# Kernel optimization log

Hardware: AMD Instinct MI355X
Metric: run time of the kernel (lower is better)

## Reference

```python
import jax, jax.numpy as jnp
import numpy as np

EPS = 1e-6
NEG = 0.2  # leaky-relu negative slope
OBJ_C = 6

def _knn(x, k):
    # x: [B,3,N] -> [B,N,k] indices of k nearest neighbors (incl. self)
    xx = jnp.sum(x * x, axis=1)
    inner = jnp.einsum('bdn,bdm->bnm', x, x)
    pd = 2.0 * inner - xx[:, :, None] - xx[:, None, :]  # negative sq dist
    return jax.lax.top_k(pd, k)[1]

def _gather_pts(xt, idx):
    # xt [B,N,D], idx [B,N,k] -> [B,N,k,D]
    return xt[jnp.arange(xt.shape[0])[:, None, None], idx]

def _vn_lin(W, x):
    # channel-mixing linear over VN channel dim: x [B,Cin,3,...]
    return jnp.einsum('oc,bc...->bo...', W, x)

def _vn_bn(x, g, b, eps=1e-5):
    # VNBatchNorm with batch statistics on vector norms
    n = jnp.linalg.norm(x, axis=2) + EPS          # [B,C,*spatial]
    axes = (0,) + tuple(range(2, n.ndim))
    m = jnp.mean(n, axes, keepdims=True)
    v = jnp.var(n, axes, keepdims=True)
    shp = (1, -1) + (1,) * (n.ndim - 2)
    nb = g.reshape(shp) * (n - m) / jnp.sqrt(v + eps) + b.reshape(shp)
    return x / n[:, :, None] * nb[:, :, None]

def _vn_leaky(p, d):
    dot = jnp.sum(p * d, axis=2, keepdims=True)
    dsq = jnp.sum(d * d, axis=2, keepdims=True)
    return NEG * p + (1.0 - NEG) * jnp.where(dot >= 0, p, p - (dot / (dsq + EPS)) * d)

def _vn_block(x, wf, wd, g=None, b=None):
    # VNLinearLeakyReLU
    p = _vn_lin(wf, x)
    if g is not None:
        p = _vn_bn(p, g, b)
    return _vn_leaky(p, _vn_lin(wd, x))

def _surface_feature(coord, k):
    # coord [B,3,N] -> [B,3(chan),3(vec),N,k]: (nb-ctr, ctr, nb x ctr)
    idx = _knn(coord, k)
    xt = coord.transpose(0, 2, 1)                                  # [B,N,3]
    nb = _gather_pts(xt, idx)[:, :, :, None, :]                    # [B,N,k,1,3]
    ctr = jnp.broadcast_to(xt[:, :, None, None, :], nb.shape)
    f = jnp.concatenate([nb - ctr, ctr, jnp.cross(nb, ctr, axis=-1)], axis=3)
    return f.transpose(0, 3, 4, 1, 2)

def _neighbor_feature(x, coord, k):
    # x [B,C,3,N], knn over coord -> [B,C,3,N,k]
    B, C, _, N = x.shape
    idx = _knn(coord, k)
    xt = x.reshape(B, C * 3, N).transpose(0, 2, 1)                 # [B,N,C*3]
    f = _gather_pts(xt, idx).reshape(B, N, k, C, 3)
    return f.transpose(0, 3, 4, 1, 2)

def _vn_maxpool_down(x, coord, wd, rate):
    # x [B,C,3,N,k]: stride-subsample points, VN-max over k neighbors
    x = x[:, :, :, ::rate, :]
    coord_d = coord[:, :, ::rate]
    dot = jnp.sum(x * _vn_lin(wd, x), axis=2)                      # [B,C,Nd,k]
    idx = jnp.argmax(dot, axis=-1)
    xm = jnp.take_along_axis(x, idx[:, :, None, :, None], axis=-1)[..., 0]
    return xm, coord_d

def _nearest_index(t, s):
    # t [B,N,3], s [B,M,3] -> argmin sq-dist index [B,N]
    d = jnp.sum(t * t, -1)[:, :, None] - 2.0 * jnp.einsum('bnd,bmd->bnm', t, s) + jnp.sum(s * s, -1)[:, None, :]
    return jnp.argmin(d, axis=-1)

def _index_points(x, idx):
    # x [B,C,3,M], idx [B,N] -> [B,C,3,N]
    xt = x.transpose(0, 3, 1, 2)
    return xt[jnp.arange(x.shape[0])[:, None], idx].transpose(0, 2, 3, 1)

def _conv_bn_relu(x, w, b, g, be, eps=1e-5):
    # 1x1 Conv1d + BatchNorm1d (batch stats) + ReLU
    y = jnp.einsum('oc,bcn->bon', w, x) + b[None, :, None]
    m = jnp.mean(y, (0, 2), keepdims=True)
    v = jnp.var(y, (0, 2), keepdims=True)
    return jax.nn.relu(g[None, :, None] * (y - m) / jnp.sqrt(v + eps) + be[None, :, None])

def _forward(x, norm, cat_id, wf0, wd0, g0, b0, wf1, wd1, g1, b1, wp1, wf2, wd2, g2, b2, wf3, wd3, g3, b3, wp2, wf4, wd4, g4, b4, wv1f, wv1d, wv2f, wv2d, w3, ws1, cb1, sg1, sb1, ws2, cb2, sg2, sb2, ws3, cb3, sg3, sb3):
    B, _, _, N = x.shape
    coord = x.reshape(B, 3, N)
    one_hot = jax.nn.one_hot(cat_id, OBJ_C, dtype=x.dtype)
    x0 = _vn_block(_surface_feature(coord, 20), wf0, wd0, g0, b0).mean(-1)   # [B,42,3,N]
    x1 = _vn_block(x0, wf1, wd1, g1, b1)
    x2, coord2 = _vn_maxpool_down(_neighbor_feature(x1, coord, 4), coord, wp1, 4)
    x2 = _vn_block(x2, wf2, wd2, g2, b2)                                     # [B,84,3,N/4]
    x3 = _vn_block(x2, wf3, wd3, g3, b3)
    x4, coord4 = _vn_maxpool_down(_neighbor_feature(x3, coord2, 4), coord2, wp2, 4)
    x4 = _vn_block(x4, wf4, wd4, g4, b4)                                     # [B,168,3,N/16]
    ct = coord.transpose(0, 2, 1)
    i1 = _nearest_index(ct, coord2.transpose(0, 2, 1))
    i2 = _nearest_index(ct, coord4.transpose(0, 2, 1))
    eqv = jnp.concatenate([x0, x1, _index_points(x2, i1), _index_points(x3, i1), _index_points(x4, i2)], axis=1)  # [B,420,3,N]
    mean_feat = eqv.mean(-1, keepdims=True)                                  # [B,420,3,1]
    z = _vn_block(mean_feat, wv1f, wv1d)
    z = _vn_block(z, wv2f, wv2d)
    z = jnp.einsum('bcvm,kc->bvkm', z, w3)                                   # [B,3,2,1]
    inv_gl = jnp.einsum('bijm,bjkm->bikm', mean_feat, z).reshape(B, -1, 1)   # [B,840,1]
    inv_0 = jnp.broadcast_to(inv_gl, (B, inv_gl.shape[1], N))
    inv_1 = jnp.sum(mean_feat * coord[:, None], axis=2)                      # [B,420,N]
    oh = jnp.broadcast_to(one_hot[:, :, None], (B, OBJ_C, N))
    inv = jnp.concatenate([norm, inv_0, inv_1, oh], axis=1)                  # [B,1267,N]
    inv = _conv_bn_relu(inv, ws1, cb1, sg1, sb1)
    inv = _conv_bn_relu(inv, ws2, cb2, sg2, sb2)
    inv = _conv_bn_relu(inv, ws3, cb3, sg3, sb3)                             # [B,420,N]
    return eqv, mean_feat, inv, inv_gl

def setup_inputs():
    key = jax.random.key(0)
    ki = iter(jax.random.split(key, 40))
    B, N, D = 4, 2048, 42
    def lin(o, c):
        return jax.random.normal(next(ki), (o, c), jnp.float32) / float(np.sqrt(c))
    inp = dict(
        x=jax.random.normal(next(ki), (B, 1, 3, N), jnp.float32),
        norm=jax.random.normal(next(ki), (B, 1, N), jnp.float32),
        cat_id=jax.random.randint(next(ki), (B,), 0, OBJ_C),
        wf0=lin(D, 3), wd0=lin(D, 3), g0=jnp.ones(D), b0=jnp.zeros(D),
        wf1=lin(D, D), wd1=lin(D, D), g1=jnp.ones(D), b1=jnp.zeros(D),
        wp1=lin(D, D),
        wf2=lin(2 * D, D), wd2=lin(2 * D, D), g2=jnp.ones(2 * D), b2=jnp.zeros(2 * D),
        wf3=lin(2 * D, 2 * D), wd3=lin(2 * D, 2 * D), g3=jnp.ones(2 * D), b3=jnp.zeros(2 * D),
        wp2=lin(2 * D, 2 * D),
        wf4=lin(4 * D, 2 * D), wd4=lin(4 * D, 2 * D), g4=jnp.ones(4 * D), b4=jnp.zeros(4 * D),
        wv1f=lin(5 * D, 10 * D), wv1d=lin(5 * D, 10 * D),
        wv2f=lin(2 * D, 5 * D), wv2d=lin(2 * D, 5 * D),
        w3=lin(2, 2 * D),
        ws1=lin(1024, 1267), cb1=jnp.zeros(1024), sg1=jnp.ones(1024), sb1=jnp.zeros(1024),
        ws2=lin(512, 1024), cb2=jnp.zeros(512), sg2=jnp.ones(512), sb2=jnp.zeros(512),
        ws3=lin(420, 512), cb3=jnp.zeros(420), sg3=jnp.ones(420), sb3=jnp.zeros(420),
    )
    return inp

def reference(x, norm, cat_id, wf0, wd0, g0, b0, wf1, wd1, g1, b1, wp1, wf2, wd2, g2, b2, wf3, wd3, g3, b3, wp2, wf4, wd4, g4, b4, wv1f, wv1d, wv2f, wv2d, w3, ws1, cb1, sg1, sb1, ws2, cb2, sg2, sb2, ws3, cb3, sg3, sb3):
    return _forward(x, norm, cat_id, wf0, wd0, g0, b0, wf1, wd1, g1, b1, wp1, wf2, wd2, g2, b2, wf3, wd3, g3, b3, wp2, wf4, wd4, g4, b4, wv1f, wv1d, wv2f, wv2d, w3, ws1, cb1, sg1, sb1, ws2, cb2, sg2, sb2, ws3, cb3, sg3, sb3)
```

## Files before the change

### kernel.cpp

```cpp
#include <hip/hip_runtime.h>
#include <hip/hip_bf16.h>
#include <cstdint>
#include <cstddef>

#define NTOT 2048
#define BTOT 4

typedef short bf16x8 __attribute__((ext_vector_type(8)));
typedef float f32x4 __attribute__((ext_vector_type(4)));

__device__ inline unsigned short f2b(float v) {
    __hip_bfloat16 h = __float2bfloat16(v);
    return *reinterpret_cast<unsigned short*>(&h);
}

static const size_t WS_IDX20 = 0;
static const size_t WS_FS    = 163840;
static const size_t WS_X0    = 1638400;
static const size_t WS_X1    = 3702784;
static const size_t WS_XM2   = 5767168;
static const size_t WS_X2    = 6025216;
static const size_t WS_X3    = 6541312;
static const size_t WS_IDX42 = 7057408;
static const size_t WS_XM4   = 7059456;
static const size_t WS_X4    = 7188480;
static const size_t WS_I1    = 7446528;
static const size_t WS_I2    = 7454720;
static const size_t WS_MF    = 7462912;
static const size_t WS_INVGL = 7467952;
static const size_t WS_STATS = 7471312;
static const size_t WS_CST   = 7472992;
static const size_t WS_CB    = 7480320;
static const size_t WS_AB    = 7484416;
static const size_t WS_W0    = 7496704;
static const size_t WS_Z1    = 7497728;
static const size_t WS_Z2    = 7500288;
static const size_t WS_W2B   = 13378560;
static const size_t WS_W3B   = 13640704;
static const size_t WS_Y1T   = 13771776;
static const size_t WS_Y1B   = 0;
static const size_t WS_Y2T   = 7480320;
static const size_t WS_Y2B   = 4194304;
static const size_t WS_Y3T   = WS_Y1T;

#define ST0_OFF 0
#define ST1_OFF 84
#define ST2_OFF 168
#define ST3_OFF 336
#define ST4_OFF 504
#define CST1_OFF 0
#define CST2_OFF 2048
#define CST3_OFF 3072

#define OUT_EQV   0
#define OUT_MF    10321920
#define OUT_INV   10326960
#define OUT_INVGL 13767600

template <int SLOTS, int K>
__global__ __launch_bounds__(256)
void knn_reg_kernel(const float* __restrict__ coord, int cand_stride, int q_stride,
                    int* __restrict__ out_idx, int q_cnt)
{
#pragma clang fp contract(off)
    constexpr int Q = SLOTS / 8;
    int b = blockIdx.y;
    int wave = threadIdx.x >> 6, lane = threadIdx.x & 63;
    int q = blockIdx.x * 4 + wave;
    if (q >= q_cnt) return;
    int nq = q * q_stride;
    float qx = coord[(b * 3 + 0) * NTOT + nq];
    float qy = coord[(b * 3 + 1) * NTOT + nq];
    float qz = coord[(b * 3 + 2) * NTOT + nq];
    float xxq = qx * qx + qy * qy + qz * qz;
    float v[SLOTS];
#pragma unroll
    for (int j = 0; j < SLOTS; ++j) {
        int mo = (lane + 64 * j) * cand_stride;
        float cx = coord[(b * 3 + 0) * NTOT + mo];
        float cy = coord[(b * 3 + 1) * NTOT + mo];
        float cz = coord[(b * 3 + 2) * NTOT + mo];
        float inner = qx * cx + qy * cy + qz * cz;
        float xxc = cx * cx + cy * cy + cz * cz;
        v[j] = (2.0f * inner - xxq) - xxc;
    }
    float qv[Q]; int qj[Q];
#pragma unroll
    for (int qq = 0; qq < Q; ++qq) {
        float nv = v[qq * 8]; int nj = qq * 8;
#pragma unroll
        for (int j = 1; j < 8; ++j)
            if (v[qq * 8 + j] > nv) { nv = v[qq * 8 + j]; nj = qq * 8 + j; }
        qv[qq] = nv; qj[qq] = nj;
    }
#pragma clang loop unroll(disable)
    for (int kk = 0; kk < K; ++kk) {
        float bv = qv[0]; int bj = qj[0];
#pragma unroll
        for (int qq = 1; qq < Q; ++qq)
            if (qv[qq] > bv) { bv = qv[qq]; bj = qj[qq]; }
        int bm = lane + 64 * bj;
        for (int off = 32; off; off >>= 1) {
            float ov = __shfl_down(bv, off);
            int   om = __shfl_down(bm, off);
            if (ov > bv || (ov == bv && om < bm)) { bv = ov; bm = om; }
        }
        int m_win = __builtin_amdgcn_readfirstlane(bm);
        if (lane == 0)
            out_idx[((size_t)(b * q_cnt) + q) * K + kk] = m_win;
        int w_slot = m_win >> 6;
        bool isw = (lane == (m_win & 63));
#pragma unroll
        for (int qq = 0; qq < Q; ++qq) {
            if (qq == (w_slot >> 3)) {
#pragma unroll
                for (int j = 0; j < 8; ++j)
                    if (qq * 8 + j == w_slot)
                        v[qq * 8 + j] = isw ? -3.4e38f : v[qq * 8 + j];
                float nv = v[qq * 8]; int nj = qq * 8;
#pragma unroll
                for (int j = 1; j < 8; ++j)
                    if (v[qq * 8 + j] > nv) { nv = v[qq * 8 + j]; nj = qq * 8 + j; }
                qv[qq] = nv; qj[qq] = nj;
            }
        }
    }
}

template <int SLOTS>
__global__ __launch_bounds__(256)
void nearest_reg_kernel(const float* __restrict__ coord, int cand_stride,
                        int* __restrict__ out)
{
#pragma clang fp contract(off)
    int b = blockIdx.y;
    int wave = threadIdx.x >> 6, lane = threadIdx.x & 63;
    int n = blockIdx.x * 4 + wave;
    float qx = coord[(b * 3 + 0) * NTOT + n];
    float qy = coord[(b * 3 + 1) * NTOT + n];
    float qz = coord[(b * 3 + 2) * NTOT + n];
    float tt = qx * qx + qy * qy + qz * qz;
    float v[SLOTS];
#pragma unroll
    for (int j = 0; j < SLOTS; ++j) {
        int mo = (lane + 64 * j) * cand_stride;
        float cx = coord[(b * 3 + 0) * NTOT + mo];
        float cy = coord[(b * 3 + 1) * NTOT + mo];
        float cz = coord[(b * 3 + 2) * NTOT + mo];
        float inner = qx * cx + qy * cy + qz * cz;
        float ss = cx * cx + cy * cy + cz * cz;
        v[j] = (tt - 2.0f * inner) + ss;
    }
    float bv = v[0];
    int bj = 0;
#pragma unroll
    for (int j = 1; j < SLOTS; ++j)
        if (v[j] < bv) { bv = v[j]; bj = j; }
    int bm = lane + 64 * bj;
    for (int off = 32; off; off >>= 1) {
        float ov = __shfl_down(bv, off);
        int   om = __shfl_down(bm, off);
        if (ov < bv || (ov == bv && om < bm)) { bv = ov; bm = om; }
    }
    if (lane == 0) out[b * NTOT + n] = bm;
}

__global__ void surf_build_kernel(const float* __restrict__ coord,
                                  const int* __restrict__ idx20,
                                  float* __restrict__ fs)
{
    int t = blockIdx.x * 256 + threadIdx.x;
    if (t >= BTOT * NTOT * 20) return;
    int n = (t / 20) & (NTOT - 1);
    int b = t / (20 * NTOT);
    int m = idx20[t];
    float cx = coord[(b * 3 + 0) * NTOT + n];
    float cy = coord[(b * 3 + 1) * NTOT + n];
    float cz = coord[(b * 3 + 2) * NTOT + n];
    float nx = coord[(b * 3 + 0) * NTOT + m];
    float ny = coord[(b * 3 + 1) * NTOT + m];
    float nz = coord[(b * 3 + 2) * NTOT + m];
    float* f9 = fs + (size_t)t * 9;
    f9[0] = nx - cx; f9[1] = ny - cy; f9[2] = nz - cz;
    f9[3] = cx;      f9[4] = cy;      f9[5] = cz;
    f9[6] = ny * cz - nz * cy;
    f9[7] = nz * cx - nx * cz;
    f9[8] = nx * cy - ny * cx;
}

__global__ __launch_bounds__(256)
void stats0_kernel(const float* __restrict__ fs,
                   const float* __restrict__ wf0,
                   double* __restrict__ stats)
{
    __shared__ float fl[6 * 180];
    __shared__ double red[2][6][42];
    int t = threadIdx.x, b = blockIdx.y;
    int ps = t / 42, o = t - ps * 42;
    bool active = ps < 6;
    float w0 = 0.f, w1 = 0.f, w2 = 0.f;
    if (active) { w0 = wf0[o * 3]; w1 = wf0[o * 3 + 1]; w2 = wf0[o * 3 + 2]; }
    double s = 0.0, s2 = 0.0;
    int base = blockIdx.x * 48;
    for (int it = 0; it < 8; ++it) {
        int n0 = base + it * 6;
        __syncthreads();
        for (int i = t; i < 1080; i += 256) {
            int pl = i / 180, off = i - pl * 180;
            int n = n0 + pl; if (n > NTOT - 1) n = NTOT - 1;
            fl[i] = fs[((size_t)(b * NTOT + n) * 20) * 9 + off];
        }
        __syncthreads();
        if (active && n0 + ps < NTOT) {
            const float* f = &fl[ps * 180];
            for (int k = 0; k < 20; ++k) {
                const float* f9 = &f[k * 9];
                float p0 = w0 * f9[0] + w1 * f9[3] + w2 * f9[6];
                float p1 = w0 * f9[1] + w1 * f9[4] + w2 * f9[7];
                float p2 = w0 * f9[2] + w1 * f9[5] + w2 * f9[8];
                float nrm = sqrtf(p0 * p0 + p1 * p1 + p2 * p2) + 1e-6f;
                s += (double)nrm; s2 += (double)nrm * (double)nrm;
            }
        }
    }
    if (active) { red[0][ps][o] = s; red[1][ps][o] = s2; }
    __syncthreads();
    if (t < 42) {
        double a = 0.0, a2 = 0.0;
#pragma unroll
        for (int p = 0; p < 6; ++p) { a += red[0][p][t]; a2 += red[1][p][t]; }
        atomicAdd(&stats[t], a);
        atomicAdd(&stats[42 + t], a2);
    }
}

__global__ __launch_bounds__(256)
void apply0_kernel(const float* __restrict__ fs,
                   const float* __restrict__ wf0,
                   const float* __restrict__ wd0,
                   const float* __restrict__ g0,
                   const float* __restrict__ b0,
                   const double* __restrict__ stats,
                   float* __restrict__ x0)
{
    __shared__ float fl[6 * 180];
    int t = threadIdx.x;
    int b = blockIdx.y;
    int ps = t / 42, o = t - ps * 42;
    int n0 = blockIdx.x * 6;
    for (int i = t; i < 1080; i += 256) {
        int pl = i / 180, off = i - pl * 180;
        int n = n0 + pl; if (n > NTOT - 1) n = NTOT - 1;
        fl[i] = fs[((size_t)(b * NTOT + n) * 20) * 9 + off];
    }
    __syncthreads();
    int n = n0 + ps;
    if (ps >= 6 || n >= NTOT) return;
    double S1 = stats[o], S2 = stats[42 + o];
    double md = S1 / 163840.0;
    float m = (float)md;
    float var = (float)(S2 / 163840.0 - md * md);
    float gs = g0[o] / sqrtf(var + 1e-5f);
    float bb = b0[o];
    float wa0 = wf0[o * 3], wa1 = wf0[o * 3 + 1], wa2 = wf0[o * 3 + 2];
    float wb0 = wd0[o * 3], wb1 = wd0[o * 3 + 1], wb2 = wd0[o * 3 + 2];
    float a0 = 0.f, a1 = 0.f, a2 = 0.f;
    const float* f = &fl[ps * 180];
    for (int k = 0; k < 20; ++k) {
        const float* f9 = &f[k * 9];
        float p0 = wa0 * f9[0] + wa1 * f9[3] + wa2 * f9[6];
        float p1 = wa0 * f9[1] + wa1 * f9[4] + wa2 * f9[7];
        float p2 = wa0 * f9[2] + wa1 * f9[5] + wa2 * f9[8];
        float d0 = wb0 * f9[0] + wb1 * f9[3] + wb2 * f9[6];
        float d1 = wb0 * f9[1] + wb1 * f9[4] + wb2 * f9[7];
        float d2 = wb0 * f9[2] + wb1 * f9[5] + wb2 * f9[8];
        float nrm = sqrtf(p0 * p0 + p1 * p1 + p2 * p2) + 1e-6f;
        float nb = gs * (nrm - m) + bb;
        float sc = nb / nrm;
        p0 *= sc; p1 *= sc; p2 *= sc;
        float dot = p0 * d0 + p1 * d1 + p2 * d2;
        float dsq = d0 * d0 + d1 * d1 + d2 * d2 + 1e-6f;
        float tq = fminf(dot, 0.f) / dsq;
        a0 += 0.2f * p0 + 0.8f * (p0 - tq * d0);
        a1 += 0.2f * p1 + 0.8f * (p1 - tq * d1);
        a2 += 0.2f * p2 + 0.8f * (p2 - tq * d2);
    }
    x0[((size_t)(b * 42 + o) * 3 + 0) * NTOT + n] = a0 / 20.0f;
    x0[((size_t)(b * 42 + o) * 3 + 1) * NTOT + n] = a1 / 20.0f;
    x0[((size_t)(b * 42 + o) * 3 + 2) * NTOT + n] = a2 / 20.0f;
}

template <int Ci, int Co, int PTS, int NT, int NIT>
__global__ __launch_bounds__(NT)
void vn_stats_kernel(const float* __restrict__ xin,
                     const float* __restrict__ wf,
                     double* __restrict__ stats, int Npts)
{
    constexpr int Ci3 = Ci * 3;
    constexpr int STRIDE = Ci3 + 1;
    __shared__ float col[PTS * STRIDE];
    __shared__ double red[2][PTS][Co];
    int t = threadIdx.x;
    int b = blockIdx.y;
    int ps = t / Co;
    int o = t - ps * Co;
    bool active = ps < PTS;
    double s = 0.0, s2 = 0.0;
    int base = blockIdx.x * (PTS * NIT);
    for (int it = 0; it < NIT; ++it) {
        int pt0 = base + it * PTS;
        __syncthreads();
        for (int i = t; i < PTS * Ci3; i += NT) {
            int pl = i / Ci3, off = i - pl * Ci3;
            int pt = pt0 + pl; if (pt >= Npts) pt = Npts - 1;
            col[pl * STRIDE + off] = xin[(size_t)(b * 3 * Ci + off) * Npts + pt];
        }
        __syncthreads();
        if (active && pt0 + ps < Npts) {
            const float* cl = &col[ps * STRIDE];
            const float* wr = wf + o * Ci;
            float p0 = 0.f, p1 = 0.f, p2 = 0.f;
#pragma unroll
            for (int c = 0; c < Ci; ++c) {
                float w = wr[c];
                p0 += w * cl[3 * c]; p1 += w * cl[3 * c + 1]; p2 += w * cl[3 * c + 2];
            }
            float nrm = sqrtf(p0 * p0 + p1 * p1 + p2 * p2) + 1e-6f;
            s += (double)nrm; s2 += (double)nrm * (double)nrm;
        }
    }
    if (active) { red[0][ps][o] = s; red[1][ps][o] = s2; }
    __syncthreads();
    if (t < Co) {
        double a = 0.0, a2 = 0.0;
#pragma unroll
        for (int p = 0; p < PTS; ++p) { a += red[0][p][t]; a2 += red[1][p][t]; }
        atomicAdd(&stats[t], a);
        atomicAdd(&stats[Co + t], a2);
    }
}

template <int Ci, int Co, int PTS, int NT>
__global__ __launch_bounds__(NT)
void vn_apply_kernel(const float* __restrict__ xin,
                     const float* __restrict__ wf,
                     const float* __restrict__ wd,
                     const float* __restrict__ g,
                     const float* __restrict__ bbp,
                     const double* __restrict__ stats,
                     double count, int Npts,
                     float* __restrict__ xout)
{
    constexpr int Ci3 = Ci * 3;
    constexpr int STRIDE = Ci3 + 1;
    __shared__ float col[PTS * STRIDE];
    int t = threadIdx.x;
    int b = blockIdx.y;
    int ps = t / Co;
    int o = t - ps * Co;
    bool active = ps < PTS;
    float m = 0.f, gs = 0.f, bb = 0.f;
// ... 193 lines not shown
    }
    if (lane == 0) {
        float dot = p0 * d0 + p1 * d1 + p2 * d2;
        float r0, r1, r2;
        if (dot >= 0.f) { r0 = p0; r1 = p1; r2 = p2; }
        else {
            float tq = dot / (d0 * d0 + d1 * d1 + d2 * d2 + 1e-6f);
            r0 = p0 - tq * d0; r1 = p1 - tq * d1; r2 = p2 - tq * d2;
        }
        z2ws[b * 252 + o * 3]     = 0.2f * p0 + 0.8f * r0;
        z2ws[b * 252 + o * 3 + 1] = 0.2f * p1 + 0.8f * r1;
        z2ws[b * 252 + o * 3 + 2] = 0.2f * p2 + 0.8f * r2;
    }
}

__global__ void z3invgl_kernel(const float* __restrict__ mfw,
                               const float* __restrict__ z2ws,
                               const float* __restrict__ w3,
                               float* __restrict__ invgl_ws,
                               float* __restrict__ out_invgl)
{
    __shared__ float z2[252];
    __shared__ float z3[6];
    __shared__ float mf[1260];
    int b = blockIdx.x;
    int t = threadIdx.x;
    for (int i = t; i < 252; i += 256) z2[i] = z2ws[b * 252 + i];
    for (int i = t; i < 1260; i += 256) mf[i] = mfw[b * 1260 + i];
    __syncthreads();
    if (t < 6) {
        int v = t / 2, kt = t % 2;
        float s = 0.f;
        for (int c = 0; c < 84; ++c) s += z2[c * 3 + v] * w3[kt * 84 + c];
        z3[v * 2 + kt] = s;
    }
    __syncthreads();
    for (int i = t; i < 840; i += 256) {
        int ii = i / 2, kt = i % 2;
        float s = mf[ii * 3] * z3[0 + kt] + mf[ii * 3 + 1] * z3[2 + kt] +
                  mf[ii * 3 + 2] * z3[4 + kt];
        invgl_ws[b * 840 + i] = s;
        out_invgl[b * 840 + i] = s;
    }
}

__global__ __launch_bounds__(256)
void conv1_coef_kernel(const float* __restrict__ ws1,
                       const float* __restrict__ invgl,
                       const float* __restrict__ mfw,
                       const int* __restrict__ cat,
                       float* __restrict__ cb, float* __restrict__ ab,
                       float* __restrict__ w0)
{
    int wave = threadIdx.x >> 6, lane = threadIdx.x & 63;
    int o = blockIdx.x * 4 + wave;
    int b = blockIdx.y;
    const float* wr = ws1 + (size_t)o * 1267;
    float s = 0.f;
    for (int j = lane; j < 840; j += 64)
        s += wr[1 + j] * invgl[b * 840 + j];
    float a0 = 0.f, a1 = 0.f, a2 = 0.f;
    for (int i = lane; i < 420; i += 64) {
        float w = wr[841 + i];
        a0 += w * mfw[b * 1260 + i * 3];
        a1 += w * mfw[b * 1260 + i * 3 + 1];
        a2 += w * mfw[b * 1260 + i * 3 + 2];
    }
    for (int off = 32; off; off >>= 1) {
        s  += __shfl_down(s, off);
        a0 += __shfl_down(a0, off);
        a1 += __shfl_down(a1, off);
        a2 += __shfl_down(a2, off);
    }
    if (lane == 0) {
        cb[b * 1024 + o] = s + wr[1261 + cat[b]];
        ab[((size_t)(b * 1024 + o)) * 3 + 0] = a0;
        ab[((size_t)(b * 1024 + o)) * 3 + 1] = a1;
        ab[((size_t)(b * 1024 + o)) * 3 + 2] = a2;
        if (b == 0) w0[o] = wr[0];
    }
}

__global__ __launch_bounds__(256)
void y1_gen_kernel(const float* __restrict__ cb, const float* __restrict__ ab,
                   const float* __restrict__ w0, const float* __restrict__ coord,
                   const float* __restrict__ normv, float* __restrict__ y1t)
{
    int pt = blockIdx.x;
    int b = pt >> 11, n = pt & 2047;
    float cx = coord[(b * 3 + 0) * NTOT + n];
    float cy = coord[(b * 3 + 1) * NTOT + n];
    float cz = coord[(b * 3 + 2) * NTOT + n];
    float nr = normv[b * NTOT + n];
    for (int it = 0; it < 4; ++it) {
        int o = it * 256 + threadIdx.x;
        size_t bo = (size_t)(b * 1024 + o);
        float v = cb[bo] + ab[bo * 3] * cx + ab[bo * 3 + 1] * cy +
                  ab[bo * 3 + 2] * cz + w0[o] * nr;
        y1t[(size_t)pt * 1024 + o] = v;
    }
}

__global__ void wconv_kernel(const float* __restrict__ src, unsigned short* __restrict__ dst,
                             int Msrc, int Ksrc, int Kpad)
{
    int k = blockIdx.x * 256 + threadIdx.x;
    int o = blockIdx.y;
    float v = (o < Msrc && k < Ksrc) ? src[(size_t)o * Ksrc + k] : 0.f;
    dst[(size_t)o * Kpad + k] = f2b(v);
}

__global__ __launch_bounds__(256)
void gemm_mfma_kernel(const unsigned short* __restrict__ A,
                      const unsigned short* __restrict__ Bw,
                      float* __restrict__ C, int K, int Mreal)
{
    __shared__ __align__(16) unsigned short Al[128 * 40];
    __shared__ __align__(16) unsigned short Bl[128 * 40];
    int t = threadIdx.x;
    int r0 = blockIdx.x * 128;
    int c0 = blockIdx.y * 128;
    int w = t >> 6, l = t & 63;
    int wm = w & 1, wn = w >> 1;
    int lm = l & 15, lq = l >> 4;
    f32x4 acc[4][4] = {};
    for (int k0 = 0; k0 < K; k0 += 32) {
        for (int half = 0; half < 2; ++half) {
            int ch = t + half * 256;
            int row = ch >> 2, kc = ch & 3;
            *(uint4*)&Al[row * 40 + kc * 8] =
                *(const uint4*)&A[(size_t)(r0 + row) * K + k0 + kc * 8];
            *(uint4*)&Bl[row * 40 + kc * 8] =
                *(const uint4*)&Bw[(size_t)(c0 + row) * K + k0 + kc * 8];
        }
        __syncthreads();
        bf16x8 af[4], bfr[4];
#pragma unroll
        for (int i = 0; i < 4; ++i)
            af[i] = *(const bf16x8*)&Al[(wm * 64 + i * 16 + lm) * 40 + lq * 8];
#pragma unroll
        for (int j = 0; j < 4; ++j)
            bfr[j] = *(const bf16x8*)&Bl[(wn * 64 + j * 16 + lm) * 40 + lq * 8];
#pragma unroll
        for (int i = 0; i < 4; ++i)
#pragma unroll
            for (int j = 0; j < 4; ++j)
                acc[i][j] = __builtin_amdgcn_mfma_f32_16x16x32_bf16(af[i], bfr[j],
                                                                    acc[i][j], 0, 0, 0);
        __syncthreads();
    }
#pragma unroll
    for (int i = 0; i < 4; ++i) {
#pragma unroll
        for (int j = 0; j < 4; ++j) {
            int col = c0 + wn * 64 + j * 16 + lm;
            if (col < Mreal) {
                int rbase = r0 + wm * 64 + i * 16 + lq * 4;
#pragma unroll
                for (int r = 0; r < 4; ++r)
                    C[(size_t)(rbase + r) * Mreal + col] = acc[i][j][r];
            }
        }
    }
}

__global__ void cstatsT_kernel(const float* __restrict__ Ct, float* __restrict__ st,
                               int Mreal)
{
    __shared__ float l1[256], l2[256];
    int t = threadIdx.x;
    int o = blockIdx.x * 64 + (t & 63);
    int r0 = blockIdx.y * 128 + (t >> 6) * 32;
    float s = 0.f, s2 = 0.f;
    if (o < Mreal) {
        for (int rr = 0; rr < 32; ++rr) {
            float v = Ct[(size_t)(r0 + rr) * Mreal + o];
            s += v; s2 += v * v;
        }
    }
    l1[t] = s; l2[t] = s2;
    __syncthreads();
    if (t < 64 && o < Mreal) {
        s  = l1[t] + l1[t + 64] + l1[t + 128] + l1[t + 192];
        s2 = l2[t] + l2[t + 64] + l2[t + 128] + l2[t + 192];
        atomicAdd(&st[o], s);
        atomicAdd(&st[Mreal + o], s2);
    }
}

__global__ void bnreluT_kernel(const float* __restrict__ Ct, const float* __restrict__ st,
                               const float* __restrict__ g, const float* __restrict__ be,
                               unsigned short* __restrict__ outb, int M, int maskM)
{
    size_t idx = (size_t)blockIdx.x * 256 + threadIdx.x;
    int o = (int)(idx & (size_t)maskM);
    float m = st[o] * (1.f / 8192.f);
    float var = st[M + o] * (1.f / 8192.f) - m * m;
    float sqv = sqrtf(var + 1e-5f);
    float v = g[o] * (Ct[idx] - m) / sqv + be[o];
    outb[idx] = f2b(v > 0.f ? v : 0.f);
}

__global__ void bnrelu_outT_kernel(const float* __restrict__ Ct, const float* __restrict__ st,
                                   const float* __restrict__ g, const float* __restrict__ be,
                                   float* __restrict__ outinv)
{
    __shared__ float tile[64][65];
    int t = threadIdx.x;
    int r0 = blockIdx.x * 64;
    int o0 = blockIdx.y * 64;
    int b = r0 >> 11, n0 = r0 & 2047;
    int oi = t & 63;
    int o = o0 + oi;
    float m = 0.f, sqv = 1.f, gg = 0.f, bb = 0.f;
    if (o < 420) {
        m = st[o] * (1.f / 8192.f);
        float var = st[420 + o] * (1.f / 8192.f) - m * m;
        sqv = sqrtf(var + 1e-5f);
        gg = g[o]; bb = be[o];
    }
    for (int it = 0; it < 16; ++it) {
        int rr = it * 4 + (t >> 6);
        float v = 0.f;
        if (o < 420) {
            v = gg * (Ct[(size_t)(r0 + rr) * 420 + o] - m) / sqv + bb;
            v = v > 0.f ? v : 0.f;
        }
        tile[rr][oi] = v;
    }
    __syncthreads();
    for (int it = 0; it < 16; ++it) {
        int oc = it * 4 + (t >> 6);
        int oo = o0 + oc;
        if (oo < 420)
            outinv[((size_t)(b * 420 + oo)) * 2048 + n0 + (t & 63)] = tile[t & 63][oc];
    }
}

extern "C" void kernel_launch(void* const* d_in, const int* in_sizes, int n_in,
                              void* d_out, int out_size, void* d_ws, size_t ws_size,
                              hipStream_t stream)
{
    (void)in_sizes; (void)n_in; (void)out_size; (void)ws_size;
    const float* xc   = (const float*)d_in[0];
    const float* normv= (const float*)d_in[1];
    const int*   cat  = (const int*)d_in[2];
    const float* wf0  = (const float*)d_in[3];
    const float* wd0  = (const float*)d_in[4];
    const float* g0   = (const float*)d_in[5];
    const float* b0   = (const float*)d_in[6];
    const float* wf1  = (const float*)d_in[7];
    const float* wd1  = (const float*)d_in[8];
    const float* g1   = (const float*)d_in[9];
    const float* b1   = (const float*)d_in[10];
    const float* wp1  = (const float*)d_in[11];
    const float* wf2  = (const float*)d_in[12];
    const float* wd2  = (const float*)d_in[13];
    const float* g2   = (const float*)d_in[14];
    const float* b2   = (const float*)d_in[15];
    const float* wf3  = (const float*)d_in[16];
    const float* wd3  = (const float*)d_in[17];
    const float* g3   = (const float*)d_in[18];
    const float* b3   = (const float*)d_in[19];
    const float* wp2  = (const float*)d_in[20];
    const float* wf4  = (const float*)d_in[21];
    const float* wd4  = (const float*)d_in[22];
    const float* g4   = (const float*)d_in[23];
    const float* b4   = (const float*)d_in[24];
    const float* wv1f = (const float*)d_in[25];
    const float* wv1d = (const float*)d_in[26];
    const float* wv2f = (const float*)d_in[27];
    const float* wv2d = (const float*)d_in[28];
    const float* w3   = (const float*)d_in[29];
    const float* ws1  = (const float*)d_in[30];
    const float* sg1  = (const float*)d_in[32];
    const float* sb1  = (const float*)d_in[33];
    const float* ws2  = (const float*)d_in[34];
    const float* sg2  = (const float*)d_in[36];
    const float* sb2  = (const float*)d_in[37];
    const float* ws3  = (const float*)d_in[38];
    const float* sg3  = (const float*)d_in[40];
    const float* sb3  = (const float*)d_in[41];

    float* ws = (float*)d_ws;
    float* out = (float*)d_out;

    int*    idx20 = (int*)(ws + WS_IDX20);
    float*  fs    = ws + WS_FS;
    float*  x0    = ws + WS_X0;
    float*  x1    = ws + WS_X1;
    float*  xm2   = ws + WS_XM2;
    float*  x2    = ws + WS_X2;
    float*  x3    = ws + WS_X3;
    int*    idx42 = (int*)(ws + WS_IDX42);
    float*  xm4   = ws + WS_XM4;
    float*  x4    = ws + WS_X4;
    int*    i1p   = (int*)(ws + WS_I1);
    int*    i2p   = (int*)(ws + WS_I2);
    float*  mfw   = ws + WS_MF;
    float*  invgl = ws + WS_INVGL;
    double* st    = (double*)(ws + WS_STATS);
    float*  cst   = ws + WS_CST;
    float*  cb    = ws + WS_CB;
    float*  ab    = ws + WS_AB;
    float*  w0    = ws + WS_W0;
    float*  z1ws  = ws + WS_Z1;
    float*  z2ws  = ws + WS_Z2;
    unsigned short* w2b  = (unsigned short*)(ws + WS_W2B);
    unsigned short* w3b  = (unsigned short*)(ws + WS_W3B);
    float*  y1t   = ws + WS_Y1T;
    unsigned short* y1b  = (unsigned short*)(ws + WS_Y1B);
    float*  y2t   = ws + WS_Y2T;
    unsigned short* y2b  = (unsigned short*)(ws + WS_Y2B);
    float*  y3t   = ws + WS_Y3T;

    hipMemsetAsync((void*)st, 0, 840 * sizeof(double), stream);
    hipMemsetAsync((void*)cst, 0, 3912 * sizeof(float), stream);
    hipMemsetAsync((void*)mfw, 0, 5040 * sizeof(float), stream);

    wconv_kernel<<<dim3(4, 512), 256, 0, stream>>>(ws2, w2b, 512, 1024, 1024);
    wconv_kernel<<<dim3(2, 512), 256, 0, stream>>>(ws3, w3b, 420, 512, 512);

    knn_reg_kernel<32, 20><<<dim3(512, 4), 256, 0, stream>>>(xc, 1, 1, idx20, 2048);
    surf_build_kernel<<<640, 256, 0, stream>>>(xc, idx20, fs);

    stats0_kernel<<<dim3(43, 4), 256, 0, stream>>>(fs, wf0, st + ST0_OFF);
    apply0_kernel<<<dim3(342, 4), 256, 0, stream>>>(fs, wf0, wd0, g0, b0,
                                                    st + ST0_OFF, x0);

    vn_stats_kernel<42, 42, 6, 256, 8><<<dim3(43, 4), 256, 0, stream>>>(
        x0, wf1, st + ST1_OFF, 2048);
    vn_apply_kernel<42, 42, 6, 256><<<dim3(342, 4), 256, 0, stream>>>(
        x0, wf1, wd1, g1, b1, st + ST1_OFF, 8192.0, 2048, x1);

    vn_pool_kernel<<<dim3(512, 4), 256, 0, stream>>>(x1, idx20, 40960LL, 80, wp1, xm2,
                                                     42, 2048, 512);
    vn_stats_kernel<42, 84, 3, 256, 8><<<dim3(22, 4), 256, 0, stream>>>(
        xm2, wf2, st + ST2_OFF, 512);
    vn_apply_kernel<42, 84, 3, 256><<<dim3(171, 4), 256, 0, stream>>>(
        xm2, wf2, wd2, g2, b2, st + ST2_OFF, 2048.0, 512, x2);
    vn_stats_kernel<84, 84, 3, 256, 8><<<dim3(22, 4), 256, 0, stream>>>(
        x2, wf3, st + ST3_OFF, 512);
    vn_apply_kernel<84, 84, 3, 256><<<dim3(171, 4), 256, 0, stream>>>(
        x2, wf3, wd3, g3, b3, st + ST3_OFF, 2048.0, 512, x3);

    knn_reg_kernel<8, 4><<<dim3(32, 4), 256, 0, stream>>>(xc, 4, 16, idx42, 128);
    vn_pool_kernel<<<dim3(128, 4), 256, 0, stream>>>(x3, idx42, 512LL, 4, wp2, xm4,
                                                     84, 512, 128);
    vn_stats_kernel<84, 168, 3, 512, 4><<<dim3(11, 4), 512, 0, stream>>>(
        xm4, wf4, st + ST4_OFF, 128);
    vn_apply_kernel<84, 168, 3, 512><<<dim3(43, 4), 512, 0, stream>>>(
        xm4, wf4, wd4, g4, b4, st + ST4_OFF, 512.0, 128, x4);

    nearest_reg_kernel<8><<<dim3(512, 4), 256, 0, stream>>>(xc, 4, i1p);
    nearest_reg_kernel<2><<<dim3(512, 4), 256, 0, stream>>>(xc, 16, i2p);

    eqv_kernel<<<dim3(8, 1260, 4), 256, 0, stream>>>(x0, x1, x2, x3, x4, i1p, i2p,
                                                     out + OUT_EQV, mfw);
    mf_finalize_kernel<<<20, 256, 0, stream>>>(mfw, out + OUT_MF);

    z1_kernel<<<dim3(53, 4), 256, 0, stream>>>(mfw, wv1f, wv1d, z1ws);
    z2_kernel<<<dim3(21, 4), 256, 0, stream>>>(z1ws, wv2f, wv2d, z2ws);
    z3invgl_kernel<<<4, 256, 0, stream>>>(mfw, z2ws, w3, invgl, out + OUT_INVGL);

    conv1_coef_kernel<<<dim3(256, 4), 256, 0, stream>>>(ws1, invgl, mfw, cat, cb, ab, w0);
    y1_gen_kernel<<<8192, 256, 0, stream>>>(cb, ab, w0, xc, normv, y1t);
    cstatsT_kernel<<<dim3(16, 64), 256, 0, stream>>>(y1t, cst + CST1_OFF, 1024);
    bnreluT_kernel<<<32768, 256, 0, stream>>>(y1t, cst + CST1_OFF, sg1, sb1, y1b,
                                              1024, 1023);

    gemm_mfma_kernel<<<dim3(64, 4), 256, 0, stream>>>(y1b, w2b, y2t, 1024, 512);
    cstatsT_kernel<<<dim3(8, 64), 256, 0, stream>>>(y2t, cst + CST2_OFF, 512);
    bnreluT_kernel<<<16384, 256, 0, stream>>>(y2t, cst + CST2_OFF, sg2, sb2, y2b,
                                              512, 511);

    gemm_mfma_kernel<<<dim3(64, 4), 256, 0, stream>>>(y2b, w3b, y3t, 512, 420);
    cstatsT_kernel<<<dim3(7, 64), 256, 0, stream>>>(y3t, cst + CST3_OFF, 420);
    bnrelu_outT_kernel<<<dim3(128, 7), 256, 0, stream>>>(y3t, cst + CST3_OFF, sg3, sb3,
                                                         out + OUT_INV);
}
```

Baseline: 643.4 us.

## Fuse surface features, y1 stats, GEMM column stats; extract top-2 per kNN round

```diff
diff --git a/kernel.cpp b/kernel.cpp
--- a/kernel.cpp
+++ b/kernel.cpp
@@ -57,6 +57,36 @@
 #define OUT_INV   10326960
 #define OUT_INVGL 13767600
 
+__device__ __forceinline__ void merge_pair(float& v1, int& m1, float& v2, int& m2,
+                                           float w1, int n1, float w2, int n2)
+{
+    bool g  = (w1 > v1) || (w1 == v1 && n1 < m1);
+    bool ga = (v1 > w2) || (v1 == w2 && m1 < n2);
+    bool gb = (w1 > v2) || (w1 == v2 && n1 < m2);
+    float s2v = g ? (ga ? v1 : w2) : (gb ? w1 : v2);
+    int   s2m = g ? (ga ? m1 : n2) : (gb ? n1 : m2);
+    float s1v = g ? w1 : v1;
+    int   s1m = g ? n1 : m1;
+    v1 = s1v; m1 = s1m; v2 = s2v; m2 = s2m;
+}
+
+__device__ __forceinline__ void qtop2(const float* v, int base,
+                                      float& a1, int& j1, float& a2, int& j2)
+{
+    a1 = v[base]; j1 = base; a2 = -3.4e38f; j2 = base;
+#pragma unroll
+    for (int j = 1; j < 8; ++j) {
+        float val = v[base + j];
+        bool b1 = val > a1;
+        bool b2 = val > a2;
+        float na2 = b1 ? a1 : (b2 ? val : a2);
+        int   nj2 = b1 ? j1 : (b2 ? base + j : j2);
+        a1 = b1 ? val : a1;
+        j1 = b1 ? base + j : j1;
+        a2 = na2; j2 = nj2;
+    }
+}
+
 template <int SLOTS, int K>
 __global__ __launch_bounds__(256)
 void knn_reg_kernel(const float* __restrict__ coord, int cand_stride, int q_stride,
@@ -84,44 +114,50 @@
         float xxc = cx * cx + cy * cy + cz * cz;
         v[j] = (2.0f * inner - xxq) - xxc;
     }
-    float qv[Q]; int qj[Q];
-#pragma unroll
-    for (int qq = 0; qq < Q; ++qq) {
-        float nv = v[qq * 8]; int nj = qq * 8;
-#pragma unroll
-        for (int j = 1; j < 8; ++j)
-            if (v[qq * 8 + j] > nv) { nv = v[qq * 8 + j]; nj = qq * 8 + j; }
-        qv[qq] = nv; qj[qq] = nj;
-    }
+    float q1v[Q], q2v[Q]; int q1j[Q], q2j[Q];
+#pragma unroll
+    for (int qq = 0; qq < Q; ++qq)
+        qtop2(v, qq * 8, q1v[qq], q1j[qq], q2v[qq], q2j[qq]);
+
 #pragma clang loop unroll(disable)
-    for (int kk = 0; kk < K; ++kk) {
-        float bv = qv[0]; int bj = qj[0];
-#pragma unroll
-        for (int qq = 1; qq < Q; ++qq)
-            if (qv[qq] > bv) { bv = qv[qq]; bj = qj[qq]; }
-        int bm = lane + 64 * bj;
+    for (int r = 0; r < K / 2; ++r) {
+        float b1v, b2v; int b1j, b2j;
+        if constexpr (Q == 4) {
+            float x1v = q1v[0], x2v = q2v[0]; int x1j = q1j[0], x2j = q2j[0];
+            merge_pair(x1v, x1j, x2v, x2j, q1v[1], q1j[1], q2v[1], q2j[1]);
+            float y1v = q1v[2], y2v = q2v[2]; int y1j = q1j[2], y2j = q2j[2];
+            merge_pair(y1v, y1j, y2v, y2j, q1v[3], q1j[3], q2v[3], q2j[3]);
+            merge_pair(x1v, x1j, x2v, x2j, y1v, y1j, y2v, y2j);
+            b1v = x1v; b1j = x1j; b2v = x2v; b2j = x2j;
+        } else {
+            b1v = q1v[0]; b1j = q1j[0]; b2v = q2v[0]; b2j = q2j[0];
+        }
+        int b1m = lane + (b1j << 6);
+        int b2m = lane + (b2j << 6);
         for (int off = 32; off; off >>= 1) {
-            float ov = __shfl_down(bv, off);
-            int   om = __shfl_down(bm, off);
-            if (ov > bv || (ov == bv && om < bm)) { bv = ov; bm = om; }
-        }
-        int m_win = __builtin_amdgcn_readfirstlane(bm);
-        if (lane == 0)
-            out_idx[((size_t)(b * q_cnt) + q) * K + kk] = m_win;
-        int w_slot = m_win >> 6;
-        bool isw = (lane == (m_win & 63));
+            float o1v = __shfl_xor(b1v, off); int o1m = __shfl_xor(b1m, off);
+            float o2v = __shfl_xor(b2v, off); int o2m = __shfl_xor(b2m, off);
+            merge_pair(b1v, b1m, b2v, b2m, o1v, o1m, o2v, o2m);
+        }
+        if (lane == 0) {
+            out_idx[((size_t)(b * q_cnt) + q) * K + 2 * r]     = b1m;
+            out_idx[((size_t)(b * q_cnt) + q) * K + 2 * r + 1] = b2m;
+        }
+        if (r == K / 2 - 1) break;
+        int ws1 = __builtin_amdgcn_readfirstlane(b1m);
+        int ws2 = __builtin_amdgcn_readfirstlane(b2m);
+        int sl1 = ws1 >> 6, sl2 = ws2 >> 6;
+        int wl1 = ws1 & 63, wl2 = ws2 & 63;
 #pragma unroll
         for (int qq = 0; qq < Q; ++qq) {
-            if (qq == (w_slot >> 3)) {
-#pragma unroll
-                for (int j = 0; j < 8; ++j)
-                    if (qq * 8 + j == w_slot)
-                        v[qq * 8 + j] = isw ? -3.4e38f : v[qq * 8 + j];
-                float nv = v[qq * 8]; int nj = qq * 8;
-#pragma unroll
-                for (int j = 1; j < 8; ++j)
-                    if (v[qq * 8 + j] > nv) { nv = v[qq * 8 + j]; nj = qq * 8 + j; }
-                qv[qq] = nv; qj[qq] = nj;
+            if ((sl1 >> 3) == qq || (sl2 >> 3) == qq) {
+#pragma unroll
+                for (int j = 0; j < 8; ++j) {
+                    int sl = qq * 8 + j;
+                    if (sl == sl1) v[sl] = (lane == wl1) ? -3.4e38f : v[sl];
+                    if (sl == sl2) v[sl] = (lane == wl2) ? -3.4e38f : v[sl];
+                }
+                qtop2(v, qq * 8, q1v[qq], q1j[qq], q2v[qq], q2j[qq]);
             }
         }
     }
@@ -165,35 +201,12 @@
     if (lane == 0) out[b * NTOT + n] = bm;
 }
 
-__global__ void surf_build_kernel(const float* __restrict__ coord,
-                                  const int* __restrict__ idx20,
-                                  float* __restrict__ fs)
-{
-    int t = blockIdx.x * 256 + threadIdx.x;
-    if (t >= BTOT * NTOT * 20) return;
-    int n = (t / 20) & (NTOT - 1);
-    int b = t / (20 * NTOT);
-    int m = idx20[t];
-    float cx = coord[(b * 3 + 0) * NTOT + n];
-    float cy = coord[(b * 3 + 1) * NTOT + n];
-    float cz = coord[(b * 3 + 2) * NTOT + n];
-    float nx = coord[(b * 3 + 0) * NTOT + m];
-    float ny = coord[(b * 3 + 1) * NTOT + m];
-    float nz = coord[(b * 3 + 2) * NTOT + m];
-    float* f9 = fs + (size_t)t * 9;
-    f9[0] = nx - cx; f9[1] = ny - cy; f9[2] = nz - cz;
-    f9[3] = cx;      f9[4] = cy;      f9[5] = cz;
-    f9[6] = ny * cz - nz * cy;
-    f9[7] = nz * cx - nx * cz;
-    f9[8] = nx * cy - ny * cx;
-}
-
 __global__ __launch_bounds__(256)
-void stats0_kernel(const float* __restrict__ fs,
-                   const float* __restrict__ wf0,
-                   double* __restrict__ stats)
-{
-    __shared__ float fl[6 * 180];
+void stats0_kernel(const float* __restrict__ coord, const int* __restrict__ idx20,
+                   const float* __restrict__ wf0, double* __restrict__ stats)
+{
+    __shared__ float nbc[360];
+    __shared__ float ctr[18];
     __shared__ double red[2][6][42];
     int t = threadIdx.x, b = blockIdx.y;
     int ps = t / 42, o = t - ps * 42;
@@ -205,19 +218,32 @@
     for (int it = 0; it < 8; ++it) {
         int n0 = base + it * 6;
         __syncthreads();
-        for (int i = t; i < 1080; i += 256) {
-            int pl = i / 180, off = i - pl * 180;
+        if (t < 120) {
+            int pl = t / 20, k = t - pl * 20;
             int n = n0 + pl; if (n > NTOT - 1) n = NTOT - 1;
-            fl[i] = fs[((size_t)(b * NTOT + n) * 20) * 9 + off];
+            int m = idx20[((size_t)(b * NTOT + n)) * 20 + k];
+            nbc[t * 3 + 0] = coord[(b * 3 + 0) * NTOT + m];
+            nbc[t * 3 + 1] = coord[(b * 3 + 1) * NTOT + m];
+            nbc[t * 3 + 2] = coord[(b * 3 + 2) * NTOT + m];
+        }
+        if (t >= 128 && t < 146) {
+            int i = t - 128; int pl = i / 3, vd = i - pl * 3;
+            int n = n0 + pl; if (n > NTOT - 1) n = NTOT - 1;
+            ctr[i] = coord[(b * 3 + vd) * NTOT + n];
         }
         __syncthreads();
         if (active && n0 + ps < NTOT) {
-            const float* f = &fl[ps * 180];
+            float cx = ctr[ps * 3], cy = ctr[ps * 3 + 1], cz = ctr[ps * 3 + 2];
+            const float* nb = &nbc[ps * 60];
             for (int k = 0; k < 20; ++k) {
-                const float* f9 = &f[k * 9];
-                float p0 = w0 * f9[0] + w1 * f9[3] + w2 * f9[6];
-                float p1 = w0 * f9[1] + w1 * f9[4] + w2 * f9[7];
-                float p2 = w0 * f9[2] + w1 * f9[5] + w2 * f9[8];
+                float nx = nb[k * 3], ny = nb[k * 3 + 1], nz = nb[k * 3 + 2];
+                float dx = nx - cx, dy = ny - cy, dz = nz - cz;
+                float crx = ny * cz - nz * cy;
+                float cry = nz * cx - nx * cz;
+                float crz = nx * cy - ny * cx;
+                float p0 = w0 * dx + w1 * cx + w2 * crx;
+                float p1 = w0 * dy + w1 * cy + w2 * cry;
+                float p2 = w0 * dz + w1 * cz + w2 * crz;
                 float nrm = sqrtf(p0 * p0 + p1 * p1 + p2 * p2) + 1e-6f;
                 s += (double)nrm; s2 += (double)nrm * (double)nrm;
             }
@@ -235,23 +261,29 @@
 }
 
 __global__ __launch_bounds__(256)
-void apply0_kernel(const float* __restrict__ fs,
-                   const float* __restrict__ wf0,
-                   const float* __restrict__ wd0,
-                   const float* __restrict__ g0,
-                   const float* __restrict__ b0,
-                   const double* __restrict__ stats,
-                   float* __restrict__ x0)
-{
-    __shared__ float fl[6 * 180];
+void apply0_kernel(const float* __restrict__ coord, const int* __restrict__ idx20,
+                   const float* __restrict__ wf0, const float* __restrict__ wd0,
+                   const float* __restrict__ g0, const float* __restrict__ b0,
+                   const double* __restrict__ stats, float* __restrict__ x0)
+{
+    __shared__ float nbc[360];
+    __shared__ float ctr[18];
     int t = threadIdx.x;
     int b = blockIdx.y;
     int ps = t / 42, o = t - ps * 42;
     int n0 = blockIdx.x * 6;
-    for (int i = t; i < 1080; i += 256) {
-        int pl = i / 180, off = i - pl * 180;
+    if (t < 120) {
+        int pl = t / 20, k = t - pl * 20;
         int n = n0 + pl; if (n > NTOT - 1) n = NTOT - 1;
-        fl[i] = fs[((size_t)(b * NTOT + n) * 20) * 9 + off];
+        int m = idx20[((size_t)(b * NTOT + n)) * 20 + k];
+        nbc[t * 3 + 0] = coord[(b * 3 + 0) * NTOT + m];
+        nbc[t * 3 + 1] = coord[(b * 3 + 1) * NTOT + m];
+        nbc[t * 3 + 2] = coord[(b * 3 + 2) * NTOT + m];
+    }
+    if (t >= 128 && t < 146) {
+        int i = t - 128; int pl = i / 3, vd = i - pl * 3;
+        int n = n0 + pl; if (n > NTOT - 1) n = NTOT - 1;
+        ctr[i] = coord[(b * 3 + vd) * NTOT + n];
     }
     __syncthreads();
     int n = n0 + ps;
@@ -264,19 +296,24 @@
     float bb = b0[o];
     float wa0 = wf0[o * 3], wa1 = wf0[o * 3 + 1], wa2 = wf0[o * 3 + 2];
     float wb0 = wd0[o * 3], wb1 = wd0[o * 3 + 1], wb2 = wd0[o * 3 + 2];
+    float cx = ctr[ps * 3], cy = ctr[ps * 3 + 1], cz = ctr[ps * 3 + 2];
+    const float* nb = &nbc[ps * 60];
     float a0 = 0.f, a1 = 0.f, a2 = 0.f;
-    const float* f = &fl[ps * 180];
     for (int k = 0; k < 20; ++k) {
-        const float* f9 = &f[k * 9];
-        float p0 = wa0 * f9[0] + wa1 * f9[3] + wa2 * f9[6];
-        float p1 = wa0 * f9[1] + wa1 * f9[4] + wa2 * f9[7];
-        float p2 = wa0 * f9[2] + wa1 * f9[5] + wa2 * f9[8];
-        float d0 = wb0 * f9[0] + wb1 * f9[3] + wb2 * f9[6];
-        float d1 = wb0 * f9[1] + wb1 * f9[4] + wb2 * f9[7];
-        float d2 = wb0 * f9[2] + wb1 * f9[5] + wb2 * f9[8];
+        float nx = nb[k * 3], ny = nb[k * 3 + 1], nz = nb[k * 3 + 2];
+        float dx = nx - cx, dy = ny - cy, dz = nz - cz;
+        float crx = ny * cz - nz * cy;
+        float cry = nz * cx - nx * cz;
+        float crz = nx * cy - ny * cx;
+        float p0 = wa0 * dx + wa1 * cx + wa2 * crx;
+        float p1 = wa0 * dy + wa1 * cy + wa2 * cry;
+        float p2 = wa0 * dz + wa1 * cz + wa2 * crz;
+        float d0 = wb0 * dx + wb1 * cx + wb2 * crx;
+        float d1 = wb0 * dy + wb1 * cy + wb2 * cry;
+        float d2 = wb0 * dz + wb1 * cz + wb2 * crz;
         float nrm = sqrtf(p0 * p0 + p1 * p1 + p2 * p2) + 1e-6f;
-        float nb = gs * (nrm - m) + bb;
-        float sc = nb / nrm;
+        float nbv = gs * (nrm - m) + bb;
+        float sc = nbv / nrm;
         p0 *= sc; p1 *= sc; p2 *= sc;
         float dot = p0 * d0 + p1 * d1 + p2 * d2;
         float dsq = d0 * d0 + d1 * d1 + d2 * d2 + 1e-6f;
@@ -636,22 +673,63 @@
 }
 
 __global__ __launch_bounds__(256)
-void y1_gen_kernel(const float* __restrict__ cb, const float* __restrict__ ab,
-                   const float* __restrict__ w0, const float* __restrict__ coord,
-                   const float* __restrict__ normv, float* __restrict__ y1t)
-{
-    int pt = blockIdx.x;
-    int b = pt >> 11, n = pt & 2047;
-    float cx = coord[(b * 3 + 0) * NTOT + n];
-    float cy = coord[(b * 3 + 1) * NTOT + n];
-    float cz = coord[(b * 3 + 2) * NTOT + n];
-    float nr = normv[b * NTOT + n];
-    for (int it = 0; it < 4; ++it) {
-        int o = it * 256 + threadIdx.x;
-        size_t bo = (size_t)(b * 1024 + o);
-        float v = cb[bo] + ab[bo * 3] * cx + ab[bo * 3 + 1] * cy +
-                  ab[bo * 3 + 2] * cz + w0[o] * nr;
-        y1t[(size_t)pt * 1024 + o] = v;
+void y1_stats_kernel(const float* __restrict__ cb, const float* __restrict__ ab,
+                     const float* __restrict__ w0, const float* __restrict__ coord,
+                     const float* __restrict__ normv, float* __restrict__ cst)
+{
+    __shared__ float px[256], py[256], pz[256], pn[256];
+    int t = threadIdx.x;
+    int o = blockIdx.x * 256 + t;
+    int b = blockIdx.y >> 3;
+    int n0 = (blockIdx.y & 7) * 256;
+    px[t] = coord[(b * 3 + 0) * NTOT + n0 + t];
+    py[t] = coord[(b * 3 + 1) * NTOT + n0 + t];
+    pz[t] = coord[(b * 3 + 2) * NTOT + n0 + t];
+    pn[t] = normv[b * NTOT + n0 + t];
+    __syncthreads();
+    size_t bo = (size_t)(b * 1024 + o);
+    float c0 = cb[bo];
+    float a0 = ab[bo * 3], a1 = ab[bo * 3 + 1], a2 = ab[bo * 3 + 2];
+    float wn = w0[o];
+    float s = 0.f, s2 = 0.f;
+    for (int k = 0; k < 256; ++k) {
+        float v = c0 + a0 * px[k] + a1 * py[k] + a2 * pz[k] + wn * pn[k];
+        s += v; s2 += v * v;
+    }
+    atomicAdd(&cst[o], s);
+    atomicAdd(&cst[1024 + o], s2);
+}
+
+__global__ __launch_bounds__(256)
+void y1_bnrelu_kernel(const float* __restrict__ cb, const float* __restrict__ ab,
+                      const float* __restrict__ w0, const float* __restrict__ coord,
+                      const float* __restrict__ normv, const float* __restrict__ cst,
+                      const float* __restrict__ sg, const float* __restrict__ sb,
+                      unsigned short* __restrict__ y1b)
+{
+    __shared__ float px[256], py[256], pz[256], pn[256];
+    int t = threadIdx.x;
+    int o = blockIdx.x * 256 + t;
+    int b = blockIdx.y >> 3;
+    int n0 = (blockIdx.y & 7) * 256;
+    px[t] = coord[(b * 3 + 0) * NTOT + n0 + t];
+    py[t] = coord[(b * 3 + 1) * NTOT + n0 + t];
+    pz[t] = coord[(b * 3 + 2) * NTOT + n0 + t];
+    pn[t] = normv[b * NTOT + n0 + t];
+    __syncthreads();
+    size_t bo = (size_t)(b * 1024 + o);
+    float c0 = cb[bo];
+    float a0 = ab[bo * 3], a1 = ab[bo * 3 + 1], a2 = ab[bo * 3 + 2];
+    float wn = w0[o];
+    float mm = cst[o] * (1.f / 8192.f);
+    float var = cst[1024 + o] * (1.f / 8192.f) - mm * mm;
+    float sc = sg[o] / sqrtf(var + 1e-5f);
+    float bs = sb[o] - mm * sc;
+    size_t rowbase = (size_t)(b * NTOT + n0) * 1024 + o;
+    for (int k = 0; k < 256; ++k) {
+        float v = c0 + a0 * px[k] + a1 * py[k] + a2 * pz[k] + wn * pn[k];
+        float r = sc * v + bs;
+        y1b[rowbase + (size_t)k * 1024] = f2b(r > 0.f ? r : 0.f);
     }
 }
 
@@ -667,11 +745,14 @@
 __global__ __launch_bounds__(256)
 void gemm_mfma_kernel(const unsigned short* __restrict__ A,
                       const unsigned short* __restrict__ Bw,
-                      float* __restrict__ C, int K, int Mreal)
+                      float* __restrict__ C, float* __restrict__ st,
+                      int K, int Mreal)
 {
     __shared__ __align__(16) unsigned short Al[128 * 40];
     __shared__ __align__(16) unsigned short Bl[128 * 40];
+    __shared__ float sst[128], sst2[128];
     int t = threadIdx.x;
+    if (t < 128) { sst[t] = 0.f; sst2[t] = 0.f; }
     int r0 = blockIdx.x * 128;
     int c0 = blockIdx.y * 128;
     int w = t >> 6, l = t & 63;
@@ -716,29 +797,28 @@
             }
         }
     }
-}
-
-__global__ void cstatsT_kernel(const float* __restrict__ Ct, float* __restrict__ st,
-                               int Mreal)
-{
-    __shared__ float l1[256], l2[256];
-    int t = threadIdx.x;
-    int o = blockIdx.x * 64 + (t & 63);
-    int r0 = blockIdx.y * 128 + (t >> 6) * 32;
-    float s = 0.f, s2 = 0.f;
-    if (o < Mreal) {
-        for (int rr = 0; rr < 32; ++rr) {
-            float v = Ct[(size_t)(r0 + rr) * Mreal + o];
-            s += v; s2 += v * v;
-        }
-    }
-    l1[t] = s; l2[t] = s2;
-    __syncthreads();
-    if (t < 64 && o < Mreal) {
-        s  = l1[t] + l1[t + 64] + l1[t + 128] + l1[t + 192];
-        s2 = l2[t] + l2[t + 64] + l2[t + 128] + l2[t + 192];
-        atomicAdd(&st[o], s);
-        atomicAdd(&st[Mreal + o], s2);
+#pragma unroll
+    for (int j = 0; j < 4; ++j) {
+        float s = 0.f, s2 = 0.f;
+#pragma unroll
+        for (int i = 0; i < 4; ++i)
+#pragma unroll
+            for (int r = 0; r < 4; ++r) { float x = acc[i][j][r]; s += x; s2 += x * x; }
+        s  += __shfl_down(s, 32);  s  += __shfl_down(s, 16);
+        s2 += __shfl_down(s2, 32); s2 += __shfl_down(s2, 16);
+        if (l < 16) {
+            int cc = wn * 64 + j * 16 + lm;
+            atomicAdd(&sst[cc], s);
+            atomicAdd(&sst2[cc], s2);
+        }
+    }
+    __syncthreads();
+    if (t < 128) {
+        int col = c0 + t;
+        if (col < Mreal) {
+            atomicAdd(&st[col], sst[t]);
+            atomicAdd(&st[Mreal + col], sst2[t]);
+        }
     }
 }
 
@@ -840,7 +920,6 @@
     float* out = (float*)d_out;
 
     int*    idx20 = (int*)(ws + WS_IDX20);
-    float*  fs    = ws + WS_FS;
     float*  x0    = ws + WS_X0;
     float*  x1    = ws + WS_X1;
     float*  xm2   = ws + WS_XM2;
@@ -862,7 +941,6 @@
     float*  z2ws  = ws + WS_Z2;
     unsigned short* w2b  = (unsigned short*)(ws + WS_W2B);
     unsigned short* w3b  = (unsigned short*)(ws + WS_W3B);
-    float*  y1t   = ws + WS_Y1T;
     unsigned short* y1b  = (unsigned short*)(ws + WS_Y1B);
     float*  y2t   = ws + WS_Y2T;
     unsigned short* y2b  = (unsigned short*)(ws + WS_Y2B);
@@ -876,10 +954,9 @@
     wconv_kernel<<<dim3(2, 512), 256, 0, stream>>>(ws3, w3b, 420, 512, 512);
 
     knn_reg_kernel<32, 20><<<dim3(512, 4), 256, 0, stream>>>(xc, 1, 1, idx20, 2048);
-    surf_build_kernel<<<640, 256, 0, stream>>>(xc, idx20, fs);
-
-    stats0_kernel<<<dim3(43, 4), 256, 0, stream>>>(fs, wf0, st + ST0_OFF);
-    apply0_kernel<<<dim3(342, 4), 256, 0, stream>>>(fs, wf0, wd0, g0, b0,
+
+    stats0_kernel<<<dim3(43, 4), 256, 0, stream>>>(xc, idx20, wf0, st + ST0_OFF);
+    apply0_kernel<<<dim3(342, 4), 256, 0, stream>>>(xc, idx20, wf0, wd0, g0, b0,
                                                     st + ST0_OFF, x0);
 
     vn_stats_kernel<42, 42, 6, 256, 8><<<dim3(43, 4), 256, 0, stream>>>(
@@ -918,18 +995,18 @@
     z3invgl_kernel<<<4, 256, 0, stream>>>(mfw, z2ws, w3, invgl, out + OUT_INVGL);
 
     conv1_coef_kernel<<<dim3(256, 4), 256, 0, stream>>>(ws1, invgl, mfw, cat, cb, ab, w0);
-    y1_gen_kernel<<<8192, 256, 0, stream>>>(cb, ab, w0, xc, normv, y1t);
-    cstatsT_kernel<<<dim3(16, 64), 256, 0, stream>>>(y1t, cst + CST1_OFF, 1024);
-    bnreluT_kernel<<<32768, 256, 0, stream>>>(y1t, cst + CST1_OFF, sg1, sb1, y1b,
-                                              1024, 1023);
-
-    gemm_mfma_kernel<<<dim3(64, 4), 256, 0, stream>>>(y1b, w2b, y2t, 1024, 512);
-    cstatsT_kernel<<<dim3(8, 64), 256, 0, stream>>>(y2t, cst + CST2_OFF, 512);
+    y1_stats_kernel<<<dim3(4, 32), 256, 0, stream>>>(cb, ab, w0, xc, normv,
+                                                     cst + CST1_OFF);
+    y1_bnrelu_kernel<<<dim3(4, 32), 256, 0, stream>>>(cb, ab, w0, xc, normv,
+                                                      cst + CST1_OFF, sg1, sb1, y1b);
+
+    gemm_mfma_kernel<<<dim3(64, 4), 256, 0, stream>>>(y1b, w2b, y2t, cst + CST2_OFF,
+                                                      1024, 512);
     bnreluT_kernel<<<16384, 256, 0, stream>>>(y2t, cst + CST2_OFF, sg2, sb2, y2b,
                                               512, 511);
 
-    gemm_mfma_kernel<<<dim3(64, 4), 256, 0, stream>>>(y2b, w3b, y3t, 512, 420);
-    cstatsT_kernel<<<dim3(7, 64), 256, 0, stream>>>(y3t, cst + CST3_OFF, 420);
+    gemm_mfma_kernel<<<dim3(64, 4), 256, 0, stream>>>(y2b, w3b, y3t, cst + CST3_OFF,
+                                                      512, 420);
     bnrelu_outT_kernel<<<dim3(128, 7), 256, 0, stream>>>(y3t, cst + CST3_OFF, sg3, sb3,
                                                          out + OUT_INV);
 }
```

Measured after the change: 643.4 us. Within noise of the previous version (-0.0%).
